# Kernel tuning notes

Measured on AMD Instinct MI355X. Metric: run time of the kernel, lower is better.

Reference implementation:

```python
import jax, jax.numpy as jnp
from jax import lax
import numpy as np

DN = ('NCHW', 'OIHW', 'NCHW')
K = 3          # deformable kernel size
DG = 4         # deform groups
EXP = 4        # InvBottle expansion


def conv_offset(x, w1, w2, b2):
    """InvBottle with diff=True: depthwise-expanded 3x3 conv, diff correction, 1x1 conv."""
    B, C, H, W = x.shape
    _x = lax.conv_general_dilated(x, w1, (1, 1), ((1, 1), (1, 1)),
                                  dimension_numbers=DN, feature_group_count=C)  # [B,4C,H,W]
    # diff_conv: subtract grouped 1x1 conv with the kernel-summed weight
    wsum = w1.sum((2, 3)).reshape(1, EXP * C, 1, 1)          # [1,4C,1,1]
    xd = _x - jnp.repeat(x, EXP, axis=1) * wsum              # group g uses input channel g
    t = lax.conv_general_dilated(xd, w2, (1, 1), ((0, 0), (0, 0)), dimension_numbers=DN)
    return t + b2.reshape(1, -1, 1, 1)                       # [B,72,H,W]


def deform_depthwise(x, off, w, pad=1):
    """Depthwise DeformConv2d (groups=C, deform_groups=DG), stride=1, dilation=1."""
    B, C, H, W = x.shape
    Cg = C // DG
    off = off.reshape(B, DG, K * K, 2, H, W)                 # (dy, dx) interleaved per tap
    dy, dx = off[:, :, :, 0], off[:, :, :, 1]                # [B,DG,9,H,W]
    ky = (jnp.arange(K * K) // K).reshape(1, 1, K * K, 1, 1).astype(x.dtype)
    kx = (jnp.arange(K * K) % K).reshape(1, 1, K * K, 1, 1).astype(x.dtype)
    py = jnp.arange(H, dtype=x.dtype).reshape(1, 1, 1, H, 1) - pad + ky + dy
    px = jnp.arange(W, dtype=x.dtype).reshape(1, 1, 1, 1, W) - pad + kx + dx

    y0 = jnp.floor(py)
    x0 = jnp.floor(px)
    wy = py - y0
    wx = px - x0

    xg = x.reshape(B, DG, Cg, H * W)

    def gather(yy, xx):
        valid = ((yy >= 0) & (yy < H) & (xx >= 0) & (xx < W)).astype(x.dtype)
        yc = jnp.clip(yy, 0, H - 1).astype(jnp.int32)
        xc = jnp.clip(xx, 0, W - 1).astype(jnp.int32)
        idx = (yc * W + xc).reshape(B, DG, 1, K * K * H * W)
        v = jnp.take_along_axis(xg, jnp.broadcast_to(idx, (B, DG, Cg, K * K * H * W)), axis=3)
        return v.reshape(B, DG, Cg, K * K, H, W) * valid[:, :, None]

    val = (gather(y0, x0) * ((1 - wy) * (1 - wx))[:, :, None]
           + gather(y0, x0 + 1) * ((1 - wy) * wx)[:, :, None]
           + gather(y0 + 1, x0) * (wy * (1 - wx))[:, :, None]
           + gather(y0 + 1, x0 + 1) * (wy * wx)[:, :, None])   # [B,DG,Cg,9,H,W]

    val = val.reshape(B, C, K * K, H, W)
    return jnp.einsum('bckhw,ck->bchw', val, w.reshape(C, K * K))


def setup_inputs() -> dict:
    key = jax.random.key(0)
    ks = jax.random.split(key, 6)
    B, C, H, W = 2, 64, 192, 192
    x1 = jax.random.normal(ks[0], (B, C, H, W), jnp.float32)
    w_off1 = jax.random.normal(ks[1], (EXP * C, 1, K, K), jnp.float32) * 0.1
    w_off2 = jax.random.normal(ks[2], (DG * 2 * K * K, EXP * C, 1, 1), jnp.float32) * 0.1
    b_off2 = jax.random.normal(ks[3], (DG * 2 * K * K,), jnp.float32) * 0.1
    w_def = jax.random.normal(ks[4], (C, 1, K, K), jnp.float32) * 0.1
    w_out = jax.random.normal(ks[5], (C, C, 1, 1), jnp.float32) * 0.1
    return {'x1': x1, 'w_off1': w_off1, 'w_off2': w_off2, 'b_off2': b_off2,
            'w_def': w_def, 'w_out': w_out}


def reference(x1, w_off1, w_off2, b_off2, w_def, w_out):
    x2 = x1
    C = x1.shape[1]
    t = conv_offset(x1, w_off1, w_off2, b_off2)              # [B,72,H,W]
    y = deform_depthwise(x1, t, w_def)                       # DeformConv2d, groups=C
    # diff_conv against the deform conv's kernel-summed depthwise weight
    y = y - x2 * w_def.sum((1, 2, 3)).reshape(1, C, 1, 1)
    m = jnp.einsum('bchw,oc->bohw', y, w_out.reshape(w_out.shape[0], C))  # 1x1, no bias
    return (x1, m)
```

## Files before the change

kernel.cpp:

```cpp
#include <hip/hip_runtime.h>

#define BN   2
#define CN   64
#define HN   192
#define WN   192
#define HWN  36864
#define OCN  256
#define JCN  72
#define SN   32

#define DROWS 8
#define XH    17
#define XW    42
#define XRT   4
#define XCL   4

typedef __attribute__((ext_vector_type(8))) short bf16x8;
typedef __attribute__((ext_vector_type(4))) float f32x4;

__device__ __forceinline__ unsigned short f2bf(float f) {
    union { float f; unsigned u; } v; v.f = f;
    unsigned r = v.u + 0x7fffu + ((v.u >> 16) & 1u);
    return (unsigned short)(r >> 16);
}

__global__ __launch_bounds__(256) void k_prep(const float* __restrict__ w2,
                                              const float* __restrict__ w_out,
                                              const float* __restrict__ w1,
                                              unsigned short* __restrict__ w2mf,
                                              unsigned short* __restrict__ w_outmf,
                                              float* __restrict__ w1p) {
    int idx = blockIdx.x * 256 + threadIdx.x;
    if (idx < 20480) {
        int j  = idx & 7;
        int l  = (idx >> 3) & 63;
        int ts = idx >> 9;
        int tm = ts >> 3, s = ts & 7;
        int jrow = tm * 16 + (l & 15);
        int k    = s * 32 + (l >> 4) * 8 + j;
        float v = (jrow < JCN) ? w2[jrow * OCN + k] : 0.f;
        w2mf[idx] = f2bf(v);
    } else if (idx < 24576) {
        int r  = idx - 20480;
        int j  = r & 7;
        int l  = (r >> 3) & 63;
        int ts = r >> 9;
        int tm = ts >> 1, s = ts & 1;
        int m  = tm * 16 + (l & 15);
        int k  = s * 32 + (l >> 4) * 8 + j;
        w_outmf[r] = f2bf(w_out[m * CN + k]);
    } else if (idx < 26624) {
        int r = idx - 24576;
        int o = r >> 3, kk = r & 7;
        int k = kk < 4 ? kk : kk + 1;
        w1p[r] = w1[o * 9 + k];
    }
}

__global__ __launch_bounds__(256, 4) void k_offsets(const float* __restrict__ x,
                                                    const float* __restrict__ w1p,
                                                    const unsigned short* __restrict__ w2mf,
                                                    const float* __restrict__ b2,
                                                    float* __restrict__ t_out,
                                                    float* __restrict__ x_copy) {
    const int tid  = threadIdx.x;
    const int wv   = tid >> 6;
    const int lane = tid & 63;
    const int q    = lane >> 4;
    const int n    = lane & 15;
    const int n0   = blockIdx.x * 64 + wv * 16;
    const int y    = blockIdx.y;
    const int b    = blockIdx.z;
    const int xcol = n0 + n;
    const float* xb = x + (size_t)b * CN * HWN;

    auto load_chunk = [&](int s, float (*ld)[9]) {
        #pragma unroll
        for (int cc = 0; cc < 2; ++cc) {
            int c = 8 * s + 2 * q + cc;
            const float* xp = xb + (size_t)c * HWN;
            #pragma unroll
            for (int k = 0; k < 9; ++k) {
                int ky = k / 3, kx = k - 3 * ky;
                int yy = y - 1 + ky, xx = xcol - 1 + kx;
                float v = 0.f;
                if ((unsigned)yy < (unsigned)HN && (unsigned)xx < (unsigned)WN)
                    v = xp[yy * WN + xx];
                ld[cc][k] = v;
            }
        }
    };

    f32x4 acc[5];
    #pragma unroll
    for (int t = 0; t < 5; ++t) acc[t] = (f32x4){0.f, 0.f, 0.f, 0.f};

    const bf16x8* ap = (const bf16x8*)w2mf + lane;

    float lbuf[2][2][9];
    load_chunk(0, lbuf[0]);
    #pragma unroll
    for (int s = 0; s < 8; ++s) {
        if (s < 7) load_chunk(s + 1, lbuf[(s + 1) & 1]);
        float (*ld)[9] = lbuf[s & 1];

        float dd[2][8];
        #pragma unroll
        for (int cc = 0; cc < 2; ++cc) {
            int c = 8 * s + 2 * q + cc;
            float ctr = ld[cc][4];
            x_copy[((size_t)b * CN + c) * HWN + y * WN + xcol] = ctr;
            #pragma unroll
            for (int kk = 0; kk < 8; ++kk) {
                int k = kk < 4 ? kk : kk + 1;
                dd[cc][kk] = ld[cc][k] - ctr;
            }
        }

        bf16x8 bfr;
        const float4* wp = (const float4*)(w1p + (size_t)(s * 32 + q * 8) * 8);
        #pragma unroll
        for (int j = 0; j < 8; ++j) {
            float4 wa = wp[2 * j];
            float4 wb = wp[2 * j + 1];
            const float* d = dd[j >> 2];
            float a = wa.x * d[0] + wa.y * d[1] + wa.z * d[2] + wa.w * d[3]
                    + wb.x * d[4] + wb.y * d[5] + wb.z * d[6] + wb.w * d[7];
            bfr[j] = (short)f2bf(a);
        }

        #pragma unroll
        for (int tm = 0; tm < 5; ++tm) {
            bf16x8 af = ap[(tm * 8 + s) * 64];
            acc[tm] = __builtin_amdgcn_mfma_f32_16x16x32_bf16(af, bfr, acc[tm], 0, 0, 0);
        }
    }

    float* tb = t_out + (size_t)b * JCN * HWN + y * WN + n0 + n;
    #pragma unroll
    for (int tm = 0; tm < 5; ++tm) {
        #pragma unroll
        for (int r = 0; r < 4; ++r) {
            int j = tm * 16 + q * 4 + r;
            if (j < JCN)
                tb[(size_t)j * HWN] = acc[tm][r] + b2[j];
        }
    }
}

__device__ __forceinline__ float dsample(const float* __restrict__ p, int yi, int xi) {
    if ((unsigned)yi < (unsigned)HN && (unsigned)xi < (unsigned)WN)
        return p[yi * WN + xi];
    return 0.f;
}

__global__ __launch_bounds__(256, 4) void k_deform(const float* __restrict__ x,
                                                   const float* __restrict__ t_in,
                                                   const float* __restrict__ wdef,
                                                   float* __restrict__ y_out) {
    __shared__ float xs[8 * XH * XW];
    __shared__ float wks[9 * 8];
    __shared__ float wsums[8];
    const int x0   = blockIdx.x * SN;
    const int yr0  = blockIdx.y * DROWS;
    const int zz   = blockIdx.z;
    const int b    = zz >> 3;
    const int chunk = zz & 7;
    const int g    = chunk >> 1;
    const int tid  = threadIdx.x;
    const int r    = tid >> 5;
    const int px   = tid & 31;
    const int row_lo = yr0 - XRT;
    const int col_lo = x0 - XCL;
    const float* xb = x + (size_t)b * CN * HWN;

    float dyr[9], dxr[9];
    {
        const float* tbp = t_in + ((size_t)b * JCN + g * 18) * HWN
                         + (yr0 + r) * WN + x0 + px;
        #pragma unroll
        for (int k = 0; k < 9; ++k) {
            dyr[k] = tbp[(size_t)(2 * k) * HWN];
            dxr[k] = tbp[(size_t)(2 * k + 1) * HWN];
        }
    }

    for (int idx = tid; idx < 8 * XH * XW; idx += 256) {
        int cc  = idx / (XH * XW);
        int rem = idx - cc * (XH * XW);
        int rr  = rem / XW;
        int col = rem - rr * XW;
        int yy  = row_lo + rr;
        int xx  = col_lo + col;
        float v = 0.f;
        if ((unsigned)yy < (unsigned)HN && (unsigned)xx < (unsigned)WN)
            v = xb[(size_t)(chunk * 8 + cc) * HWN + yy * WN + xx];
        xs[idx] = v;
    }
    if (tid < 72) {
        int k = tid >> 3, cc = tid & 7;
        wks[tid] = wdef[(chunk * 8 + cc) * 9 + k];
    } else if (tid < 80) {
        int cc = tid - 72;
        float s = 0.f;
        #pragma unroll
        for (int k = 0; k < 9; ++k) s += wdef[(chunk * 8 + cc) * 9 + k];
        wsums[cc] = s;
    }
    __syncthreads();

    float acc[8];
    #pragma unroll
    for (int c = 0; c < 8; ++c)
        acc[c] = -xs[c * (XH * XW) + (XRT + r) * XW + XCL + px] * wsums[c];

    const float ry_basef = (float)(yr0 + r - 1);
    const float rx_basef = (float)(x0 + px - 1);

    #pragma unroll
    for (int k = 0; k < 9; ++k) {
        const int ky = k / 3, kx = k - 3 * ky;
        float py  = ry_basef + (float)ky + dyr[k];
        float pxf = rx_basef + (float)kx + dxr[k];
        float y0f = floorf(py), x0f = floorf(pxf);
        float wy = py - y0f, wx = pxf - x0f;
        int yi = (int)y0f, xi = (int)x0f;
        int ry = yi - row_lo, rx = xi - col_lo;
        float omwy = 1.f - wy, omwx = 1.f - wx;
        float w00 = omwy * omwx;
        float w01 = omwy * wx;
        float w10 = wy * omwx;
        float w11 = wy * wx;
        float4 wka = *(const float4*)&wks[k * 8];
        float4 wkb = *(const float4*)&wks[k * 8 + 4];
        float wkv[8] = {wka.x, wka.y, wka.z, wka.w, wkb.x, wkb.y, wkb.z, wkb.w};
        if ((unsigned)ry < (XH - 1) && (unsigned)rx < (XW - 1)) {
            const float* p0 = xs + ry * XW + rx;
            #pragma unroll
            for (int c = 0; c < 8; ++c) {
                const float* p = p0 + c * (XH * XW);
                float bil = p[0] * w00 + p[1] * w01 + p[XW] * w10 + p[XW + 1] * w11;
                acc[c] += wkv[c] * bil;
            }
        } else {
            #pragma unroll
            for (int c = 0; c < 8; ++c) {
                const float* xp = xb + (size_t)(chunk * 8 + c) * HWN;
                float v00 = dsample(xp, yi,     xi);
                float v01 = dsample(xp, yi,     xi + 1);
                float v10 = dsample(xp, yi + 1, xi);
                float v11 = dsample(xp, yi + 1, xi + 1);
                float bil = v00 * w00 + v01 * w01 + v10 * w10 + v11 * w11;
                acc[c] += wkv[c] * bil;
            }
        }
    }

    float* yo = y_out + ((size_t)b * CN + chunk * 8) * HWN + (yr0 + r) * WN + x0 + px;
    #pragma unroll
    for (int c = 0; c < 8; ++c)
        yo[(size_t)c * HWN] = acc[c];
}

__global__ __launch_bounds__(256, 8) void k_final(const float* __restrict__ y_in,
                                                  const unsigned short* __restrict__ womf,
                                                  float* __restrict__ m_out) {
    const int tid  = threadIdx.x;
    const int wv   = tid >> 6;
    const int lane = tid & 63;
    const int q    = lane >> 4;
    const int n    = lane & 15;
    const int n0   = blockIdx.x * 64 + wv * 16;
    const int yr   = blockIdx.y;
    const int b    = blockIdx.z;

    const float* yb = y_in + (size_t)b * CN * HWN + yr * WN + n0 + n;

    float yv[2][8];
    #pragma unroll
    for (int s = 0; s < 2; ++s)
        #pragma unroll
        for (int j = 0; j < 8; ++j)
            yv[s][j] = yb[(size_t)(s * 32 + q * 8 + j) * HWN];

    bf16x8 bfr[2];
    #pragma unroll
    for (int s = 0; s < 2; ++s)
        #pragma unroll
        for (int j = 0; j < 8; ++j)
            bfr[s][j] = (short)f2bf(yv[s][j]);

    const bf16x8* ap = (const bf16x8*)womf + lane;
    f32x4 acc[4];
    #pragma unroll
    for (int tm = 0; tm < 4; ++tm) acc[tm] = (f32x4){0.f, 0.f, 0.f, 0.f};
    #pragma unroll
    for (int tm = 0; tm < 4; ++tm) {
        #pragma unroll
        for (int s = 0; s < 2; ++s) {
            bf16x8 af = ap[(tm * 2 + s) * 64];
            acc[tm] = __builtin_amdgcn_mfma_f32_16x16x32_bf16(af, bfr[s], acc[tm], 0, 0, 0);
        }
    }

    float* mb = m_out + (size_t)b * CN * HWN + yr * WN + n0 + n;
    #pragma unroll
    for (int tm = 0; tm < 4; ++tm) {
        #pragma unroll
        for (int r = 0; r < 4; ++r)
            mb[(size_t)(tm * 16 + q * 4 + r) * HWN] = acc[tm][r];
    }
}

extern "C" void kernel_launch(void* const* d_in, const int* in_sizes, int n_in,
                              void* d_out, int out_size, void* d_ws, size_t ws_size,
                              hipStream_t stream) {
    const float* x1    = (const float*)d_in[0];
    const float* w_off1 = (const float*)d_in[1];
    const float* w_off2 = (const float*)d_in[2];
    const float* b_off2 = (const float*)d_in[3];
    const float* w_def = (const float*)d_in[4];
    const float* w_out = (const float*)d_in[5];

    float* out = (float*)d_out;
    const size_t n_x = (size_t)BN * CN * HWN;
    float* out_x1 = out;
    float* out_m  = out + n_x;

    char* ws0 = (char*)d_ws;
    unsigned short* w2mf   = (unsigned short*)ws0;
    unsigned short* w_outmf = (unsigned short*)(ws0 + 40960);
    float* w1p    = (float*)(ws0 + 49152);
    float* t_ws   = (float*)(ws0 + 57344);
    float* y_ws   = t_ws + (size_t)BN * JCN * HWN;

    dim3 blk(256);

    k_prep<<<dim3(104), blk, 0, stream>>>(w_off2, w_out, w_off1, w2mf, w_outmf, w1p);
    k_offsets<<<dim3(WN / 64, HN, BN), blk, 0, stream>>>(x1, w1p, w2mf, b_off2,
                                                         t_ws, out_x1);
    k_deform<<<dim3(WN / SN, HN / DROWS, BN * 8), blk, 0, stream>>>(x1, t_ws, w_def, y_ws);
    k_final<<<dim3(WN / 64, HN, BN), blk, 0, stream>>>(y_ws, w_outmf, out_m);
}
```

Before: 180.3 us.

## Fuse deformable depthwise conv with 1x1 output MFMA conv via shared memory

Merges the deform kernel and the final 1x1 conv into one kernel. Each block handles a 4x16 pixel tile across all 64 channels, looping over the 4 deform groups. It stages a 16-channel halo tile per group in LDS and writes bf16 results into a shared buffer that feeds the MFMA. This removes the fp32 y intermediate round trip through global memory and one launch. In exchange, the halo tiles are smaller, so more halo is loaded per output and the global-memory fallback path is taken more often, with extra syncs per group.

```diff
diff --git a/kernel.cpp b/kernel.cpp
--- a/kernel.cpp
+++ b/kernel.cpp
@@ -7,16 +7,17 @@
 #define HWN  36864
 #define OCN  256
 #define JCN  72
-#define SN   32
-
-#define DROWS 8
-#define XH    17
-#define XW    42
-#define XRT   4
-#define XCL   4
+
+#define TR   4
+#define TC   16
+#define TPX  64
+#define GH   13
+#define GW   26
+#define GSZ  (GH * GW)
 
 typedef __attribute__((ext_vector_type(8))) short bf16x8;
 typedef __attribute__((ext_vector_type(4))) float f32x4;
+typedef __attribute__((ext_vector_type(4))) unsigned short u16x4;
 
 __device__ __forceinline__ unsigned short f2bf(float f) {
     union { float f; unsigned u; } v; v.f = f;
@@ -154,161 +155,155 @@
     return 0.f;
 }
 
-__global__ __launch_bounds__(256, 4) void k_deform(const float* __restrict__ x,
-                                                   const float* __restrict__ t_in,
-                                                   const float* __restrict__ wdef,
-                                                   float* __restrict__ y_out) {
-    __shared__ float xs[8 * XH * XW];
-    __shared__ float wks[9 * 8];
-    __shared__ float wsums[8];
-    const int x0   = blockIdx.x * SN;
-    const int yr0  = blockIdx.y * DROWS;
-    const int zz   = blockIdx.z;
-    const int b    = zz >> 3;
-    const int chunk = zz & 7;
-    const int g    = chunk >> 1;
-    const int tid  = threadIdx.x;
-    const int r    = tid >> 5;
-    const int px   = tid & 31;
-    const int row_lo = yr0 - XRT;
-    const int col_lo = x0 - XCL;
+__global__ __launch_bounds__(256, 4) void k_def_final(const float* __restrict__ x,
+                                                      const float* __restrict__ t_in,
+                                                      const float* __restrict__ wdef,
+                                                      const unsigned short* __restrict__ womf,
+                                                      float* __restrict__ m_out) {
+    __shared__ float xs[16 * GSZ];
+    __shared__ unsigned short ybuf[TPX * 72];
+    __shared__ float wks[9 * 64];
+    __shared__ float wsums[64];
+
+    const int tid = threadIdx.x;
+    const int x0  = blockIdx.x * TC;
+    const int yr0 = blockIdx.y * TR;
+    const int b   = blockIdx.z;
+    const int p   = tid & 63;
+    const int cp  = tid >> 6;
+    const int rr  = p >> 4;
+    const int cc  = p & 15;
+    const int row_lo = yr0 - 4;
+    const int col_lo = x0 - 4;
     const float* xb = x + (size_t)b * CN * HWN;
 
-    float dyr[9], dxr[9];
-    {
-        const float* tbp = t_in + ((size_t)b * JCN + g * 18) * HWN
-                         + (yr0 + r) * WN + x0 + px;
+    for (int i = tid; i < 576; i += 256)
+        wks[i] = wdef[(i & 63) * 9 + (i >> 6)];
+    if (tid < 64) {
+        float s = 0.f;
+        #pragma unroll
+        for (int k = 0; k < 9; ++k) s += wdef[tid * 9 + k];
+        wsums[tid] = s;
+    }
+
+    const int sch = tid >> 4;
+    const int sc  = tid & 15;
+    const float ry_basef = (float)(yr0 + rr - 1);
+    const float rx_basef = (float)(x0 + cc - 1);
+
+    for (int g = 0; g < 4; ++g) {
+        float dyr[9], dxr[9];
+        {
+            const float* tbp = t_in + ((size_t)b * JCN + g * 18) * HWN
+                             + (yr0 + rr) * WN + x0 + cc;
+            #pragma unroll
+            for (int k = 0; k < 9; ++k) {
+                dyr[k] = tbp[(size_t)(2 * k) * HWN];
+                dxr[k] = tbp[(size_t)(2 * k + 1) * HWN];
+            }
+        }
+
+        {
+            const float* xp = xb + (size_t)(g * 16 + sch) * HWN;
+            float* xd = xs + sch * GSZ;
+            for (int r2 = 0; r2 < GH; ++r2) {
+                int yy = row_lo + r2;
+                bool yok = (unsigned)yy < (unsigned)HN;
+                int rowoff = yy * WN;
+                #pragma unroll
+                for (int h = 0; h < 2; ++h) {
+                    int c2 = sc + h * 16;
+                    if (c2 < GW) {
+                        int xx = col_lo + c2;
+                        float v = 0.f;
+                        if (yok && (unsigned)xx < (unsigned)WN)
+                            v = xp[rowoff + xx];
+                        xd[r2 * GW + c2] = v;
+                    }
+                }
+            }
+        }
+        __syncthreads();
+
+        const int cbase = g * 16 + cp * 4;
+        float acc[4];
+        {
+            f32x4 ws4 = *(const f32x4*)&wsums[cbase];
+            const float* ctr = xs + (cp * 4) * GSZ + (rr + 4) * GW + (cc + 4);
+            #pragma unroll
+            for (int i = 0; i < 4; ++i)
+                acc[i] = -ctr[i * GSZ] * ws4[i];
+        }
+
         #pragma unroll
         for (int k = 0; k < 9; ++k) {
-            dyr[k] = tbp[(size_t)(2 * k) * HWN];
-            dxr[k] = tbp[(size_t)(2 * k + 1) * HWN];
-        }
-    }
-
-    for (int idx = tid; idx < 8 * XH * XW; idx += 256) {
-        int cc  = idx / (XH * XW);
-        int rem = idx - cc * (XH * XW);
-        int rr  = rem / XW;
-        int col = rem - rr * XW;
-        int yy  = row_lo + rr;
-        int xx  = col_lo + col;
-        float v = 0.f;
-        if ((unsigned)yy < (unsigned)HN && (unsigned)xx < (unsigned)WN)
-            v = xb[(size_t)(chunk * 8 + cc) * HWN + yy * WN + xx];
-        xs[idx] = v;
-    }
-    if (tid < 72) {
-        int k = tid >> 3, cc = tid & 7;
-        wks[tid] = wdef[(chunk * 8 + cc) * 9 + k];
-    } else if (tid < 80) {
-        int cc = tid - 72;
-        float s = 0.f;
-        #pragma unroll
-        for (int k = 0; k < 9; ++k) s += wdef[(chunk * 8 + cc) * 9 + k];
-        wsums[cc] = s;
-    }
-    __syncthreads();
-
-    float acc[8];
-    #pragma unroll
-    for (int c = 0; c < 8; ++c)
-        acc[c] = -xs[c * (XH * XW) + (XRT + r) * XW + XCL + px] * wsums[c];
-
-    const float ry_basef = (float)(yr0 + r - 1);
-    const float rx_basef = (float)(x0 + px - 1);
-
-    #pragma unroll
-    for (int k = 0; k < 9; ++k) {
-        const int ky = k / 3, kx = k - 3 * ky;
-        float py  = ry_basef + (float)ky + dyr[k];
-        float pxf = rx_basef + (float)kx + dxr[k];
-        float y0f = floorf(py), x0f = floorf(pxf);
-        float wy = py - y0f, wx = pxf - x0f;
-        int yi = (int)y0f, xi = (int)x0f;
-        int ry = yi - row_lo, rx = xi - col_lo;
-        float omwy = 1.f - wy, omwx = 1.f - wx;
-        float w00 = omwy * omwx;
-        float w01 = omwy * wx;
-        float w10 = wy * omwx;
-        float w11 = wy * wx;
-        float4 wka = *(const float4*)&wks[k * 8];
-        float4 wkb = *(const float4*)&wks[k * 8 + 4];
-        float wkv[8] = {wka.x, wka.y, wka.z, wka.w, wkb.x, wkb.y, wkb.z, wkb.w};
-        if ((unsigned)ry < (XH - 1) && (unsigned)rx < (XW - 1)) {
-            const float* p0 = xs + ry * XW + rx;
-            #pragma unroll
-            for (int c = 0; c < 8; ++c) {
-                const float* p = p0 + c * (XH * XW);
-                float bil = p[0] * w00 + p[1] * w01 + p[XW] * w10 + p[XW + 1] * w11;
-                acc[c] += wkv[c] * bil;
-            }
-        } else {
-            #pragma unroll
-            for (int c = 0; c < 8; ++c) {
-                const float* xp = xb + (size_t)(chunk * 8 + c) * HWN;
-                float v00 = dsample(xp, yi,     xi);
-                float v01 = dsample(xp, yi,     xi + 1);
-                float v10 = dsample(xp, yi + 1, xi);
-                float v11 = dsample(xp, yi + 1, xi + 1);
-                float bil = v00 * w00 + v01 * w01 + v10 * w10 + v11 * w11;
-                acc[c] += wkv[c] * bil;
-            }
-        }
-    }
-
-    float* yo = y_out + ((size_t)b * CN + chunk * 8) * HWN + (yr0 + r) * WN + x0 + px;
-    #pragma unroll
-    for (int c = 0; c < 8; ++c)
-        yo[(size_t)c * HWN] = acc[c];
-}
-
-__global__ __launch_bounds__(256, 8) void k_final(const float* __restrict__ y_in,
-                                                  const unsigned short* __restrict__ womf,
-                                                  float* __restrict__ m_out) {
-    const int tid  = threadIdx.x;
-    const int wv   = tid >> 6;
+            const int ky = k / 3, kx = k - 3 * ky;
+            float py  = ry_basef + (float)ky + dyr[k];
+            float pxf = rx_basef + (float)kx + dxr[k];
+            float y0f = floorf(py), x0f = floorf(pxf);
+            float wy = py - y0f, wx = pxf - x0f;
+            int yi = (int)y0f, xi = (int)x0f;
+            int ry = yi - row_lo, rx = xi - col_lo;
+            float omwy = 1.f - wy, omwx = 1.f - wx;
+            float w00 = omwy * omwx;
+            float w01 = omwy * wx;
+            float w10 = wy * omwx;
+            float w11 = wy * wx;
+            f32x4 wk4 = *(const f32x4*)&wks[k * 64 + cbase];
+            if ((unsigned)ry < (GH - 1) && (unsigned)rx < (GW - 1)) {
+                const float* p0 = xs + (cp * 4) * GSZ + ry * GW + rx;
+                #pragma unroll
+                for (int i = 0; i < 4; ++i) {
+                    const float* pp = p0 + i * GSZ;
+                    float bil = pp[0] * w00 + pp[1] * w01 + pp[GW] * w10 + pp[GW + 1] * w11;
+                    acc[i] += wk4[i] * bil;
+                }
+            } else {
+                #pragma unroll
+                for (int i = 0; i < 4; ++i) {
+                    const float* xp = xb + (size_t)(cbase + i) * HWN;
+                    float v00 = dsample(xp, yi,     xi);
+                    float v01 = dsample(xp, yi,     xi + 1);
+                    float v10 = dsample(xp, yi + 1, xi);
+                    float v11 = dsample(xp, yi + 1, xi + 1);
+                    float bil = v00 * w00 + v01 * w01 + v10 * w10 + v11 * w11;
+                    acc[i] += wk4[i] * bil;
+                }
+            }
+        }
+
+        u16x4 pk;
+        #pragma unroll
+        for (int i = 0; i < 4; ++i) pk[i] = f2bf(acc[i]);
+        *(u16x4*)&ybuf[p * 72 + cbase] = pk;
+        __syncthreads();
+    }
+
     const int lane = tid & 63;
     const int q    = lane >> 4;
     const int n    = lane & 15;
-    const int n0   = blockIdx.x * 64 + wv * 16;
-    const int yr   = blockIdx.y;
-    const int b    = blockIdx.z;
-
-    const float* yb = y_in + (size_t)b * CN * HWN + yr * WN + n0 + n;
-
-    float yv[2][8];
-    #pragma unroll
-    for (int s = 0; s < 2; ++s)
-        #pragma unroll
-        for (int j = 0; j < 8; ++j)
-            yv[s][j] = yb[(size_t)(s * 32 + q * 8 + j) * HWN];
-
-    bf16x8 bfr[2];
-    #pragma unroll
-    for (int s = 0; s < 2; ++s)
-        #pragma unroll
-        for (int j = 0; j < 8; ++j)
-            bfr[s][j] = (short)f2bf(yv[s][j]);
+    const int wv   = tid >> 6;
+
+    const unsigned short* yrow = &ybuf[(wv * 16 + n) * 72];
+    bf16x8 bfr0 = *(const bf16x8*)&yrow[q * 8];
+    bf16x8 bfr1 = *(const bf16x8*)&yrow[32 + q * 8];
 
     const bf16x8* ap = (const bf16x8*)womf + lane;
-    f32x4 acc[4];
-    #pragma unroll
-    for (int tm = 0; tm < 4; ++tm) acc[tm] = (f32x4){0.f, 0.f, 0.f, 0.f};
+    f32x4 mc[4];
+    #pragma unroll
+    for (int tm = 0; tm < 4; ++tm) mc[tm] = (f32x4){0.f, 0.f, 0.f, 0.f};
     #pragma unroll
     for (int tm = 0; tm < 4; ++tm) {
-        #pragma unroll
-        for (int s = 0; s < 2; ++s) {
-            bf16x8 af = ap[(tm * 2 + s) * 64];
-            acc[tm] = __builtin_amdgcn_mfma_f32_16x16x32_bf16(af, bfr[s], acc[tm], 0, 0, 0);
-        }
-    }
-
-    float* mb = m_out + (size_t)b * CN * HWN + yr * WN + n0 + n;
+        mc[tm] = __builtin_amdgcn_mfma_f32_16x16x32_bf16(ap[(tm * 2 + 0) * 64], bfr0, mc[tm], 0, 0, 0);
+        mc[tm] = __builtin_amdgcn_mfma_f32_16x16x32_bf16(ap[(tm * 2 + 1) * 64], bfr1, mc[tm], 0, 0, 0);
+    }
+
+    float* mb = m_out + (size_t)b * CN * HWN + (size_t)(yr0 + wv) * WN + x0 + n;
     #pragma unroll
     for (int tm = 0; tm < 4; ++tm) {
         #pragma unroll
         for (int r = 0; r < 4; ++r)
-            mb[(size_t)(tm * 16 + q * 4 + r) * HWN] = acc[tm][r];
+            mb[(size_t)(tm * 16 + q * 4 + r) * HWN] = mc[tm][r];
     }
 }
 
@@ -332,13 +327,12 @@
     unsigned short* w_outmf = (unsigned short*)(ws0 + 40960);
     float* w1p    = (float*)(ws0 + 49152);
     float* t_ws   = (float*)(ws0 + 57344);
-    float* y_ws   = t_ws + (size_t)BN * JCN * HWN;
 
     dim3 blk(256);
 
     k_prep<<<dim3(104), blk, 0, stream>>>(w_off2, w_out, w_off1, w2mf, w_outmf, w1p);
     k_offsets<<<dim3(WN / 64, HN, BN), blk, 0, stream>>>(x1, w1p, w2mf, b_off2,
                                                          t_ws, out_x1);
-    k_deform<<<dim3(WN / SN, HN / DROWS, BN * 8), blk, 0, stream>>>(x1, t_ws, w_def, y_ws);
-    k_final<<<dim3(WN / 64, HN, BN), blk, 0, stream>>>(y_ws, w_outmf, out_m);
-}
+    k_def_final<<<dim3(WN / TC, HN / TR, BN), blk, 0, stream>>>(x1, t_ws, w_def,
+                                                                w_outmf, out_m);
+}
```

New measurement: 258.2 us. +43.2%, slower.

## Store deform output as packed bf16 MFMA tiles and remap blocks for XCD locality

Applied to the files above, without the earlier changes.

k_deform now converts its 8 channel accumulators to bf16 and writes them as one 16-byte vector, in a layout that k_final can load directly as MFMA B fragments. This halves the intermediate y traffic and replaces many strided scalar loads with two vector loads per lane. Both k_offsets and k_deform also remap their linear block IDs so that neighbouring tiles land on the same XCD, aiming for better L2 reuse of x and the offset maps. The bf16 rounding happens at the same point as before, so accuracy is unchanged. The hard-coded remap constants tie the code to this exact grid shape.

```diff
diff --git a/kernel.cpp b/kernel.cpp
--- a/kernel.cpp
+++ b/kernel.cpp
@@ -15,7 +15,10 @@
 #define XRT   4
 #define XCL   4
 
+#define PGRPS 2304
+
 typedef __attribute__((ext_vector_type(8))) short bf16x8;
+typedef __attribute__((ext_vector_type(8))) unsigned short u16x8;
 typedef __attribute__((ext_vector_type(4))) float f32x4;
 
 __device__ __forceinline__ unsigned short f2bf(float f) {
@@ -63,14 +66,20 @@
                                                     const float* __restrict__ b2,
                                                     float* __restrict__ t_out,
                                                     float* __restrict__ x_copy) {
+    const int f  = blockIdx.x + 3 * blockIdx.y + 576 * blockIdx.z;
+    const int nn = (f & 7) * 144 + (f >> 3);
+    const int bx = nn % 3;
+    const int by = (nn / 3) % 192;
+    const int bz = nn / 576;
+
     const int tid  = threadIdx.x;
     const int wv   = tid >> 6;
     const int lane = tid & 63;
     const int q    = lane >> 4;
     const int n    = lane & 15;
-    const int n0   = blockIdx.x * 64 + wv * 16;
-    const int y    = blockIdx.y;
-    const int b    = blockIdx.z;
+    const int n0   = bx * 64 + wv * 16;
+    const int y    = by;
+    const int b    = bz;
     const int xcol = n0 + n;
     const float* xb = x + (size_t)b * CN * HWN;
 
@@ -157,13 +166,22 @@
 __global__ __launch_bounds__(256, 4) void k_deform(const float* __restrict__ x,
                                                    const float* __restrict__ t_in,
                                                    const float* __restrict__ wdef,
-                                                   float* __restrict__ y_out) {
+                                                   unsigned short* __restrict__ y_out) {
     __shared__ float xs[8 * XH * XW];
     __shared__ float wks[9 * 8];
     __shared__ float wsums[8];
-    const int x0   = blockIdx.x * SN;
-    const int yr0  = blockIdx.y * DROWS;
-    const int zz   = blockIdx.z;
+
+    const int f    = blockIdx.x + 6 * blockIdx.y + 144 * blockIdx.z;
+    const int slot = f >> 3;
+    const int xcd  = f & 7;
+    const int tile = slot >> 1;
+    const int cm   = slot & 1;
+    const int zz   = 2 * xcd + cm;
+    const int bx   = tile % 6;
+    const int byy  = tile / 6;
+
+    const int x0   = bx * SN;
+    const int yr0  = byy * DROWS;
     const int b    = zz >> 3;
     const int chunk = zz & 7;
     const int g    = chunk >> 1;
@@ -256,13 +274,17 @@
         }
     }
 
-    float* yo = y_out + ((size_t)b * CN + chunk * 8) * HWN + (yr0 + r) * WN + x0 + px;
-    #pragma unroll
-    for (int c = 0; c < 8; ++c)
-        yo[(size_t)c * HWN] = acc[c];
-}
-
-__global__ __launch_bounds__(256, 8) void k_final(const float* __restrict__ y_in,
+    u16x8 pk;
+    #pragma unroll
+    for (int c = 0; c < 8; ++c) pk[c] = f2bf(acc[c]);
+    const int P = (yr0 + r) * (WN / 16) + ((x0 + px) >> 4);
+    unsigned short* yo = y_out
+        + ((((size_t)b * PGRPS + P) * 2 + (chunk >> 2)) * 4 + (chunk & 3)) * 128
+        + (px & 15) * 8;
+    *(u16x8*)yo = pk;
+}
+
+__global__ __launch_bounds__(256, 8) void k_final(const unsigned short* __restrict__ y_bf,
                                                   const unsigned short* __restrict__ womf,
                                                   float* __restrict__ m_out) {
     const int tid  = threadIdx.x;
@@ -270,25 +292,13 @@
     const int lane = tid & 63;
     const int q    = lane >> 4;
     const int n    = lane & 15;
-    const int n0   = blockIdx.x * 64 + wv * 16;
     const int yr   = blockIdx.y;
     const int b    = blockIdx.z;
-
-    const float* yb = y_in + (size_t)b * CN * HWN + yr * WN + n0 + n;
-
-    float yv[2][8];
-    #pragma unroll
-    for (int s = 0; s < 2; ++s)
-        #pragma unroll
-        for (int j = 0; j < 8; ++j)
-            yv[s][j] = yb[(size_t)(s * 32 + q * 8 + j) * HWN];
-
-    bf16x8 bfr[2];
-    #pragma unroll
-    for (int s = 0; s < 2; ++s)
-        #pragma unroll
-        for (int j = 0; j < 8; ++j)
-            bfr[s][j] = (short)f2bf(yv[s][j]);
+    const int P    = yr * (WN / 16) + blockIdx.x * 4 + wv;
+
+    const unsigned short* yp = y_bf + ((size_t)b * PGRPS + P) * 1024;
+    bf16x8 bfr0 = *(const bf16x8*)(yp + (0 * 64 + q * 16 + n) * 8);
+    bf16x8 bfr1 = *(const bf16x8*)(yp + (1 * 64 + q * 16 + n) * 8);
 
     const bf16x8* ap = (const bf16x8*)womf + lane;
     f32x4 acc[4];
@@ -296,14 +306,11 @@
     for (int tm = 0; tm < 4; ++tm) acc[tm] = (f32x4){0.f, 0.f, 0.f, 0.f};
     #pragma unroll
     for (int tm = 0; tm < 4; ++tm) {
-        #pragma unroll
-        for (int s = 0; s < 2; ++s) {
-            bf16x8 af = ap[(tm * 2 + s) * 64];
-            acc[tm] = __builtin_amdgcn_mfma_f32_16x16x32_bf16(af, bfr[s], acc[tm], 0, 0, 0);
-        }
-    }
-
-    float* mb = m_out + (size_t)b * CN * HWN + yr * WN + n0 + n;
+        acc[tm] = __builtin_amdgcn_mfma_f32_16x16x32_bf16(ap[(tm * 2 + 0) * 64], bfr0, acc[tm], 0, 0, 0);
+        acc[tm] = __builtin_amdgcn_mfma_f32_16x16x32_bf16(ap[(tm * 2 + 1) * 64], bfr1, acc[tm], 0, 0, 0);
+    }
+
+    float* mb = m_out + (size_t)b * CN * HWN + yr * WN + blockIdx.x * 64 + wv * 16 + n;
     #pragma unroll
     for (int tm = 0; tm < 4; ++tm) {
         #pragma unroll
@@ -332,13 +339,13 @@
     unsigned short* w_outmf = (unsigned short*)(ws0 + 40960);
     float* w1p    = (float*)(ws0 + 49152);
     float* t_ws   = (float*)(ws0 + 57344);
-    float* y_ws   = t_ws + (size_t)BN * JCN * HWN;
+    unsigned short* y_bf = (unsigned short*)(ws0 + 57344 + 21233664);
 
     dim3 blk(256);
 
     k_prep<<<dim3(104), blk, 0, stream>>>(w_off2, w_out, w_off1, w2mf, w_outmf, w1p);
     k_offsets<<<dim3(WN / 64, HN, BN), blk, 0, stream>>>(x1, w1p, w2mf, b_off2,
                                                          t_ws, out_x1);
-    k_deform<<<dim3(WN / SN, HN / DROWS, BN * 8), blk, 0, stream>>>(x1, t_ws, w_def, y_ws);
-    k_final<<<dim3(WN / 64, HN, BN), blk, 0, stream>>>(y_ws, w_outmf, out_m);
-}
+    k_deform<<<dim3(WN / SN, HN / DROWS, BN * 8), blk, 0, stream>>>(x1, t_ws, w_def, y_bf);
+    k_final<<<dim3(WN / 64, HN, BN), blk, 0, stream>>>(y_bf, w_outmf, out_m);
+}
```

Result: faster. 170.1 us (-5.7%).
